# Kernel tuning notes

Hardware: AMD Instinct MI355X
Metric: run time of the kernel (lower is better)

## Reference

```python
import jax, jax.numpy as jnp
import numpy as np

KERNEL_SIZE = 65
STRIDE = 1
PAD = (KERNEL_SIZE - 1) // 2  # padding='same'


def setup_inputs() -> dict:
    key = jax.random.key(0)
    k1, k2 = jax.random.split(key)
    B, Cin, T = 8, 512, 512
    out_size = (Cin + 2 * PAD - (KERNEL_SIZE - 1) - 1) // STRIDE + 1  # 512
    x = jax.random.normal(k1, (B, Cin, T), dtype=jnp.float32)
    # per-output-position weights, init randn/sqrt(K) as in the torch module
    weights = jax.random.normal(k2, (out_size, 1, KERNEL_SIZE), dtype=jnp.float32) / jnp.sqrt(
        jnp.float32(KERNEL_SIZE)
    )
    bias = jnp.zeros((out_size, 1), dtype=jnp.float32)
    return {"x": x, "weights": weights, "bias": bias}


def reference(x, weights, bias):
    # x: (B, Cin, T) -> output (B, T, out_size)
    out_size, _, K = weights.shape
    xt = jnp.swapaxes(x, 1, 2)                       # (B, T, Cin)
    xp = jnp.pad(xt, ((0, 0), (0, 0), (PAD, PAD)))   # (B, T, Cin + 2p)
    # sliding windows over the (padded) channel axis: (out_size, K) gather indices
    idx = jnp.arange(out_size)[:, None] * STRIDE + jnp.arange(K)[None, :]
    win = xp[:, :, idx]                              # (B, T, out_size, K)
    # locally-connected matvec: distinct K-vector per output position o
    y = jnp.einsum("btok,ok->bto", win, weights[:, 0, :])
    y = y + bias[:, 0]                               # (B, T, out_size)
    return y
```

## Files before the change

kernel.cpp:

```cpp
#include <hip/hip_runtime.h>

#define B_    8
#define C_    512
#define T_    512
#define O_    512
#define K_    65
#define PAD_  32

#define O_TILE 32
#define T_TILE 128
#define J_     8
#define NW     4
#define ROWS   (O_TILE + 2 * PAD_)
#define NR     (J_ + 2 * PAD_)
#define YPITCH 36

#define XTILE_ELEMS (ROWS * T_TILE)
#define WT_TILE     (NW * NR * J_)
#define NOG        (O_ / J_)
#define WT_ELEMS   (NOG * NR * J_)

__global__ __launch_bounds__(256) void wt_prep(const float* __restrict__ w,
                                               float* __restrict__ wt) {
    int e = blockIdx.x * 256 + threadIdx.x;
    if (e >= WT_ELEMS) return;
    int og  = e / (NR * J_);
    int rem = e % (NR * J_);
    int r   = rem >> 3;
    int j   = rem & 7;
    int k   = r - j;
    float v = 0.0f;
    if (k >= 0 && k < K_) v = w[(og * J_ + j) * K_ + k];
    wt[e] = v;
}

template <bool USE_WS>
__global__ __launch_bounds__(256, 2)
void conv_main(const float* __restrict__ x,
               const float* __restrict__ w,
               const float* __restrict__ wt,
               const float* __restrict__ bias,
               float* __restrict__ out) {
    __shared__ float smem[XTILE_ELEMS + (USE_WS ? 0 : WT_TILE)];
    float* xs = smem;

    const int tid = threadIdx.x;
    const int bid = blockIdx.x;
    const int b   = bid >> 6;
    const int rem = bid & 63;
    const int ob  = rem >> 2;
    const int tb  = rem & 3;
    const int t0  = tb * T_TILE;
    const int c_base = ob * O_TILE - PAD_;

    {
        const float* xb = x + (size_t)b * (C_ * T_);
        const int l32 = tid & 31;
        const int rg  = tid >> 5;
        #pragma unroll
        for (int rr = 0; rr < ROWS / 8; ++rr) {
            const int row = rr * 8 + rg;
            const int c   = c_base + row;
            float4 v = make_float4(0.f, 0.f, 0.f, 0.f);
            if (c >= 0 && c < C_)
                v = *(const float4*)(xb + c * T_ + t0 + l32 * 4);
            *(float4*)(&xs[row * T_TILE + l32 * 4]) = v;
        }
    }

    if (!USE_WS) {
        float* wts = smem + XTILE_ELEMS;
        #pragma unroll
        for (int p = 0; p < WT_TILE / 256; ++p) {
            const int e  = p * 256 + tid;
            const int wg = e / (NR * J_);
            const int r2 = e % (NR * J_);
            const int r  = r2 >> 3;
            const int j  = r2 & 7;
            const int o  = (ob * NW + wg) * J_ + j;
            const int k  = r - j;
            float v = 0.f;
            if (k >= 0 && k < K_) v = w[o * K_ + k];
            wts[e] = v;
        }
    }
    __syncthreads();

    const int lane  = tid & 63;
    const int wu    = __builtin_amdgcn_readfirstlane(tid >> 6);
    const int og    = ob * NW + wu;
    const int obase = og * J_;

    float2 acc[J_];
    #pragma unroll
    for (int j = 0; j < J_; ++j) {
        const float bj = bias[obase + j];
        acc[j] = make_float2(bj, bj);
    }

    const int tl = lane * 2;
    const float* xrow = xs + (wu * J_) * T_TILE + tl;
    const float4* wrow = USE_WS
        ? (const float4*)(wt + (size_t)og * (NR * J_))
        : (const float4*)(smem + XTILE_ELEMS + wu * (NR * J_));

    #pragma unroll 8
    for (int r = 0; r < NR; ++r) {
        const float2 xv = *(const float2*)(xrow + r * T_TILE);
        const float4 wa = wrow[2 * r];
        const float4 wb = wrow[2 * r + 1];
        acc[0].x += wa.x * xv.x;  acc[0].y += wa.x * xv.y;
        acc[1].x += wa.y * xv.x;  acc[1].y += wa.y * xv.y;
        acc[2].x += wa.z * xv.x;  acc[2].y += wa.z * xv.y;
        acc[3].x += wa.w * xv.x;  acc[3].y += wa.w * xv.y;
        acc[4].x += wb.x * xv.x;  acc[4].y += wb.x * xv.y;
        acc[5].x += wb.y * xv.x;  acc[5].y += wb.y * xv.y;
        acc[6].x += wb.z * xv.x;  acc[6].y += wb.z * xv.y;
        acc[7].x += wb.w * xv.x;  acc[7].y += wb.w * xv.y;
    }

    __syncthreads();

    {
        const int olb = wu * J_;
        *(float4*)(&smem[tl * YPITCH + olb])           = make_float4(acc[0].x, acc[1].x, acc[2].x, acc[3].x);
        *(float4*)(&smem[tl * YPITCH + olb + 4])       = make_float4(acc[4].x, acc[5].x, acc[6].x, acc[7].x);
        *(float4*)(&smem[(tl + 1) * YPITCH + olb])     = make_float4(acc[0].y, acc[1].y, acc[2].y, acc[3].y);
        *(float4*)(&smem[(tl + 1) * YPITCH + olb + 4]) = make_float4(acc[4].y, acc[5].y, acc[6].y, acc[7].y);
    }
    __syncthreads();

    {
        float* ob_out = out + (size_t)b * (T_ * O_) + (size_t)t0 * O_ + ob * O_TILE;
        const int ol   = (tid & 7) * 4;
        const int trow = tid >> 3;
        #pragma unroll
        for (int p = 0; p < 4; ++p) {
            const int t_local = p * 32 + trow;
            const float4 v = *(const float4*)(&smem[t_local * YPITCH + ol]);
            *(float4*)(ob_out + (size_t)t_local * O_ + ol) = v;
        }
    }
}

extern "C" void kernel_launch(void* const* d_in, const int* in_sizes, int n_in,
                              void* d_out, int out_size, void* d_ws, size_t ws_size,
                              hipStream_t stream) {
    const float* x    = (const float*)d_in[0];
    const float* w    = (const float*)d_in[1];
    const float* bias = (const float*)d_in[2];
    float* out = (float*)d_out;
    float* wt  = (float*)d_ws;

    const int nblocks = B_ * (O_ / O_TILE) * (T_ / T_TILE);

    if (ws_size >= (size_t)WT_ELEMS * sizeof(float)) {
        wt_prep<<<(WT_ELEMS + 255) / 256, 256, 0, stream>>>(w, wt);
        conv_main<true><<<nblocks, 256, 0, stream>>>(x, w, wt, bias, out);
    } else {
        conv_main<false><<<nblocks, 256, 0, stream>>>(x, w, w, bias, out);
    }
}
```

Before: 74.29 us.

## Fuse weight prep into one kernel with 8 waves of 4 outputs each

Removes the separate weight-transposition kernel and its global workspace round trip. The banded weight tile is now built in shared memory inside the main kernel. Blocks grow from 4 to 8 waves, each wave covering 4 output channels instead of 8. This cuts a kernel launch and raises thread-level parallelism per tile. In exchange each thread does less reuse per x load, and each block pays the cost of building the weights.

Result: no change. 73.41 us (-1.2%).

```diff
diff --git a/kernel.cpp b/kernel.cpp
--- a/kernel.cpp
+++ b/kernel.cpp
@@ -9,40 +9,24 @@
 
 #define O_TILE 32
 #define T_TILE 128
-#define J_     8
-#define NW     4
+#define J_     4
+#define NWAVE  8
+#define NTHR   512
 #define ROWS   (O_TILE + 2 * PAD_)
-#define NR     (J_ + 2 * PAD_)
+#define NR_    (J_ + 2 * PAD_)
 #define YPITCH 36
 
 #define XTILE_ELEMS (ROWS * T_TILE)
-#define WT_TILE     (NW * NR * J_)
-#define NOG        (O_ / J_)
-#define WT_ELEMS   (NOG * NR * J_)
+#define WT_TILE     (NWAVE * NR_ * J_)
 
-__global__ __launch_bounds__(256) void wt_prep(const float* __restrict__ w,
-                                               float* __restrict__ wt) {
-    int e = blockIdx.x * 256 + threadIdx.x;
-    if (e >= WT_ELEMS) return;
-    int og  = e / (NR * J_);
-    int rem = e % (NR * J_);
-    int r   = rem >> 3;
-    int j   = rem & 7;
-    int k   = r - j;
-    float v = 0.0f;
-    if (k >= 0 && k < K_) v = w[(og * J_ + j) * K_ + k];
-    wt[e] = v;
-}
-
-template <bool USE_WS>
-__global__ __launch_bounds__(256, 2)
-void conv_main(const float* __restrict__ x,
-               const float* __restrict__ w,
-               const float* __restrict__ wt,
-               const float* __restrict__ bias,
-               float* __restrict__ out) {
-    __shared__ float smem[XTILE_ELEMS + (USE_WS ? 0 : WT_TILE)];
-    float* xs = smem;
+__global__ __launch_bounds__(NTHR, 4)
+void conv_fused(const float* __restrict__ x,
+                const float* __restrict__ w,
+                const float* __restrict__ bias,
+                float* __restrict__ out) {
+    __shared__ float smem[XTILE_ELEMS + WT_TILE];
+    float* xs  = smem;
+    float* wts = smem + XTILE_ELEMS;
 
     const int tid = threadIdx.x;
     const int bid = blockIdx.x;
@@ -58,8 +42,8 @@
         const int l32 = tid & 31;
         const int rg  = tid >> 5;
         #pragma unroll
-        for (int rr = 0; rr < ROWS / 8; ++rr) {
-            const int row = rr * 8 + rg;
+        for (int rr = 0; rr < ROWS / 16; ++rr) {
+            const int row = rr * 16 + rg;
             const int c   = c_base + row;
             float4 v = make_float4(0.f, 0.f, 0.f, 0.f);
             if (c >= 0 && c < C_)
@@ -68,28 +52,28 @@
         }
     }
 
-    if (!USE_WS) {
-        float* wts = smem + XTILE_ELEMS;
+    {
         #pragma unroll
-        for (int p = 0; p < WT_TILE / 256; ++p) {
-            const int e  = p * 256 + tid;
-            const int wg = e / (NR * J_);
-            const int r2 = e % (NR * J_);
-            const int r  = r2 >> 3;
-            const int j  = r2 & 7;
-            const int o  = (ob * NW + wg) * J_ + j;
-            const int k  = r - j;
-            float v = 0.f;
-            if (k >= 0 && k < K_) v = w[o * K_ + k];
-            wts[e] = v;
+        for (int p = 0; p < (WT_TILE + NTHR - 1) / NTHR; ++p) {
+            const int e = p * NTHR + tid;
+            if (e < WT_TILE) {
+                const int g  = e / (NR_ * J_);
+                const int r2 = e % (NR_ * J_);
+                const int r  = r2 >> 2;
+                const int j  = r2 & 3;
+                const int o  = (ob * NWAVE + g) * J_ + j;
+                const int k  = r - j;
+                float v = 0.f;
+                if (k >= 0 && k < K_) v = w[o * K_ + k];
+                wts[e] = v;
+            }
         }
     }
     __syncthreads();
 
-    const int lane  = tid & 63;
-    const int wu    = __builtin_amdgcn_readfirstlane(tid >> 6);
-    const int og    = ob * NW + wu;
-    const int obase = og * J_;
+    const int lane = tid & 63;
+    const int wu   = __builtin_amdgcn_readfirstlane(tid >> 6);
+    const int obase = ob * O_TILE + wu * J_;
 
     float2 acc[J_];
     #pragma unroll
@@ -100,34 +84,22 @@
 
     const int tl = lane * 2;
     const float* xrow = xs + (wu * J_) * T_TILE + tl;
-    const float4* wrow = USE_WS
-        ? (const float4*)(wt + (size_t)og * (NR * J_))
-        : (const float4*)(smem + XTILE_ELEMS + wu * (NR * J_));
+    const float4* wrow = (const float4*)(wts) + wu * NR_;
 
-    #pragma unroll 8
-    for (int r = 0; r < NR; ++r) {
+    #pragma unroll 4
+    for (int r = 0; r < NR_; ++r) {
         const float2 xv = *(const float2*)(xrow + r * T_TILE);
-        const float4 wa = wrow[2 * r];
-        const float4 wb = wrow[2 * r + 1];
-        acc[0].x += wa.x * xv.x;  acc[0].y += wa.x * xv.y;
-        acc[1].x += wa.y * xv.x;  acc[1].y += wa.y * xv.y;
-        acc[2].x += wa.z * xv.x;  acc[2].y += wa.z * xv.y;
-        acc[3].x += wa.w * xv.x;  acc[3].y += wa.w * xv.y;
-        acc[4].x += wb.x * xv.x;  acc[4].y += wb.x * xv.y;
-        acc[5].x += wb.y * xv.x;  acc[5].y += wb.y * xv.y;
-        acc[6].x += wb.z * xv.x;  acc[6].y += wb.z * xv.y;
-        acc[7].x += wb.w * xv.x;  acc[7].y += wb.w * xv.y;
+        const float4 wv = wrow[r];
+        acc[0].x += wv.x * xv.x;  acc[0].y += wv.x * xv.y;
+        acc[1].x += wv.y * xv.x;  acc[1].y += wv.y * xv.y;
+        acc[2].x += wv.z * xv.x;  acc[2].y += wv.z * xv.y;
+        acc[3].x += wv.w * xv.x;  acc[3].y += wv.w * xv.y;
     }
 
     __syncthreads();
 
-    {
-        const int olb = wu * J_;
-        *(float4*)(&smem[tl * YPITCH + olb])           = make_float4(acc[0].x, acc[1].x, acc[2].x, acc[3].x);
-        *(float4*)(&smem[tl * YPITCH + olb + 4])       = make_float4(acc[4].x, acc[5].x, acc[6].x, acc[7].x);
-        *(float4*)(&smem[(tl + 1) * YPITCH + olb])     = make_float4(acc[0].y, acc[1].y, acc[2].y, acc[3].y);
-        *(float4*)(&smem[(tl + 1) * YPITCH + olb + 4]) = make_float4(acc[4].y, acc[5].y, acc[6].y, acc[7].y);
-    }
+    *(float4*)(&smem[tl * YPITCH + wu * J_])       = make_float4(acc[0].x, acc[1].x, acc[2].x, acc[3].x);
+    *(float4*)(&smem[(tl + 1) * YPITCH + wu * J_]) = make_float4(acc[0].y, acc[1].y, acc[2].y, acc[3].y);
     __syncthreads();
 
     {
@@ -135,8 +107,8 @@
         const int ol   = (tid & 7) * 4;
         const int trow = tid >> 3;
         #pragma unroll
-        for (int p = 0; p < 4; ++p) {
-            const int t_local = p * 32 + trow;
+        for (int p = 0; p < 2; ++p) {
+            const int t_local = p * 64 + trow;
             const float4 v = *(const float4*)(&smem[t_local * YPITCH + ol]);
             *(float4*)(ob_out + (size_t)t_local * O_ + ol) = v;
         }
@@ -150,14 +122,8 @@
     const float* w    = (const float*)d_in[1];
     const float* bias = (const float*)d_in[2];
     float* out = (float*)d_out;
-    float* wt  = (float*)d_ws;
+    (void)d_ws; (void)ws_size;
 
     const int nblocks = B_ * (O_ / O_TILE) * (T_ / T_TILE);
-
-    if (ws_size >= (size_t)WT_ELEMS * sizeof(float)) {
-        wt_prep<<<(WT_ELEMS + 255) / 256, 256, 0, stream>>>(w, wt);
-        conv_main<true><<<nblocks, 256, 0, stream>>>(x, w, wt, bias, out);
-    } else {
-        conv_main<false><<<nblocks, 256, 0, stream>>>(x, w, w, bias, out);
-    }
+    conv_fused<<<nblocks, NTHR, 0, stream>>>(x, w, bias, out);
 }
```
